# Optimization experiments

Measured on AMD Instinct MI355X. Metric: run time of the kernel, lower is better.

The kernel has to match this reference:

```python
import math
import jax, jax.numpy as jnp
import numpy as np

EMBED_DIM = 1024
NUM_HEADS = 16
HEAD_DIM = EMBED_DIM // NUM_HEADS
NUM_BUCKETS = 32
MAX_DISTANCE = 128


def _relative_position_bucket(relative_position, num_buckets=NUM_BUCKETS, max_distance=MAX_DISTANCE):
    # Bidirectional T5 bucketing (matches torch reference exactly).
    num_buckets = num_buckets // 2
    relative_buckets = (relative_position > 0).astype(jnp.int32) * num_buckets
    relative_position = jnp.abs(relative_position)
    max_exact = num_buckets // 2
    is_small = relative_position < max_exact
    rp_large = jnp.log(relative_position.astype(jnp.float32) / max_exact) / math.log(max_distance / max_exact)
    rp_large = max_exact + (rp_large * (num_buckets - max_exact)).astype(jnp.int32)
    rp_large = jnp.minimum(rp_large, num_buckets - 1)
    relative_buckets = relative_buckets + jnp.where(is_small, relative_position, rp_large)
    return relative_buckets


def compute_bias(rel_emb, query_length, key_length):
    context_position = jnp.arange(query_length, dtype=jnp.int32)[:, None]
    memory_position = jnp.arange(key_length, dtype=jnp.int32)[None, :]
    relative_position = memory_position - context_position  # [q, k]
    buckets = _relative_position_bucket(relative_position)
    values = rel_emb[buckets]                 # [q, k, h]
    return jnp.transpose(values, (2, 0, 1))[None]  # [1, h, q, k]


def setup_inputs() -> dict:
    key = jax.random.key(0)
    k1, k2, k3, k4 = jax.random.split(key, 4)
    B, S = 2, 2048
    hidden_states = jax.random.normal(k1, (B, S, EMBED_DIM), dtype=jnp.float32)
    scale = 1.0 / math.sqrt(EMBED_DIM)
    W_qkv = jax.random.normal(k2, (EMBED_DIM, 3 * EMBED_DIM), dtype=jnp.float32) * scale
    W_out = jax.random.normal(k3, (EMBED_DIM, EMBED_DIM), dtype=jnp.float32) * scale
    rel_emb = jax.random.normal(k4, (NUM_BUCKETS, NUM_HEADS), dtype=jnp.float32) * 0.02
    return {"hidden_states": hidden_states, "W_qkv": W_qkv, "W_out": W_out, "rel_emb": rel_emb}


def reference(hidden_states, W_qkv, W_out, rel_emb):
    B, S, _ = hidden_states.shape
    qkv = hidden_states @ W_qkv                                # [B, S, 3*D]
    qkv = qkv.reshape(B, S, 3, NUM_HEADS, HEAD_DIM)
    qkv = jnp.transpose(qkv, (0, 3, 2, 1, 4))                  # [B, H, 3, S, dh]
    q, k, v = qkv[:, :, 0], qkv[:, :, 1], qkv[:, :, 2]
    scores = jnp.einsum('bhqd,bhkd->bhqk', q, k)               # no 1/sqrt(d) scaling (T5 style)
    scores = scores + compute_bias(rel_emb, S, S)
    attn = jax.nn.softmax(scores.astype(jnp.float32), axis=-1).astype(scores.dtype)
    out = jnp.einsum('bhqk,bhkd->bhqd', attn, v)               # [B, H, S, dh]
    out = jnp.transpose(out, (0, 2, 1, 3)).reshape(B, S, EMBED_DIM)
    return out @ W_out
```

## Files before the change

### kernel.cpp

```cpp
#include <hip/hip_runtime.h>
#include <hip/hip_bf16.h>
#include <math.h>

typedef _Float16 f16;
typedef __attribute__((ext_vector_type(8))) _Float16 f16x8;
typedef __attribute__((ext_vector_type(4))) _Float16 f16x4;
typedef __attribute__((ext_vector_type(2))) _Float16 f16x2;
typedef __attribute__((ext_vector_type(4))) float f32x4;

#define EMBED 1024
#define NHEADS 16
#define HDIM 64
#define BATCH 2
#define SEQ 2048
#define BS 4096
#define LOG2E 1.4426950408889634f


__device__ __forceinline__ f32x4 mfma16x32(f16x8 a, f16x8 b, f32x4 c) {
  return __builtin_amdgcn_mfma_f32_16x16x32_f16(a, b, c, 0, 0, 0);
}
__device__ __forceinline__ f16x2 cvt_pk(float a, float b) {
  return __builtin_bit_cast(f16x2, __builtin_amdgcn_cvt_pkrtz(a, b));
}
__device__ __forceinline__ void gload_lds16(const f16* __restrict__ g, f16* l) {
  __builtin_amdgcn_global_load_lds(
      (const __attribute__((address_space(1))) void*)g,
      (__attribute__((address_space(3))) void*)l, 16, 0, 0);
}

__global__ void prep_kernel(const float* __restrict__ X, const float* __restrict__ Wqkv,
                            const float* __restrict__ Wout, const float* __restrict__ rel_emb,
                            f16* __restrict__ Xh, f16* __restrict__ Wqkv_t,
                            f16* __restrict__ Wout_t, float* __restrict__ btab) {
  __shared__ float tile[32][33];
  int bid = blockIdx.x, tid = threadIdx.x;
  if (bid < 4096) {
    int i = (bid * 256 + tid) * 4;
    float4 v = *(const float4*)(X + i);
    f16x4 o = { (f16)v.x, (f16)v.y, (f16)v.z, (f16)v.w };
    *(f16x4*)(Xh + i) = o;
  } else if (bid < 8192) {
    const float* in;
    f16* out;
    int N, idx;
    if (bid < 7168) { in = Wqkv; out = Wqkv_t; N = 3072; idx = bid - 4096; }
    else            { in = Wout; out = Wout_t; N = 1024; idx = bid - 7168; }
    int nt = N / 32;
    int n0 = (idx % nt) * 32, k0 = (idx / nt) * 32;
    int tx = tid & 31, ty = tid >> 5;
#pragma unroll
    for (int r = ty; r < 32; r += 8) tile[r][tx] = in[(size_t)(k0 + r) * N + n0 + tx];
    __syncthreads();
#pragma unroll
    for (int r = ty; r < 32; r += 8) out[(size_t)(n0 + r) * 1024 + k0 + tx] = (f16)tile[tx][r];
  } else {
    int idx = (bid - 8192) * 256 + tid;
    if (idx >= 4095) return;
    int rp = idx - 2047;
    int rb = rp > 0 ? 16 : 0;
    int arp = rp < 0 ? -rp : rp;
    int loc;
    if (arp < 8) {
      loc = arp;
    } else {
      float lr = logf((float)arp * 0.125f) * (1.0f / 2.7725887222397811f);
      int t = 8 + (int)(lr * 8.0f);
      loc = t < 15 ? t : 15;
    }
    int bucket = rb + loc;
#pragma unroll
    for (int h = 0; h < 16; h++) btab[h * 4095 + idx] = rel_emb[bucket * 16 + h] * LOG2E;
  }
}

__device__ __forceinline__ void gemm_core(const f16* __restrict__ A, const f16* __restrict__ Bt,
                                          int m0, int n0, int Kdim, f32x4 (&acc)[4][4]) {
  __shared__ __align__(16) f16 As[128 * 32];
  __shared__ __align__(16) f16 Bs[128 * 32];

  int tid = threadIdx.x;
  int lane = tid & 63, wave = tid >> 6;
  int l15 = lane & 15, quad = lane >> 4;
  int wr = (wave >> 1) * 64, wc = (wave & 1) * 64;
  int rowl = lane >> 2;
  int col8 = (lane & 3) * 8;

#pragma unroll
  for (int i = 0; i < 4; i++)
#pragma unroll
    for (int j = 0; j < 4; j++) acc[i][j] = f32x4{0.f, 0.f, 0.f, 0.f};

  for (int kt = 0; kt < Kdim / 32; kt++) {
    int kk = kt * 32;
#pragma unroll
    for (int c = 0; c < 2; c++) {
      int row = wave * 32 + c * 16 + rowl;
      gload_lds16(A + (size_t)(m0 + row) * Kdim + kk + col8, &As[(wave * 32 + c * 16) * 32]);
      gload_lds16(Bt + (size_t)(n0 + row) * Kdim + kk + col8, &Bs[(wave * 32 + c * 16) * 32]);
    }
    __syncthreads();
    f16x8 af[4], bf[4];
#pragma unroll
    for (int i = 0; i < 4; i++) af[i] = *(const f16x8*)(&As[(wr + i * 16 + l15) * 32 + quad * 8]);
#pragma unroll
    for (int j = 0; j < 4; j++) bf[j] = *(const f16x8*)(&Bs[(wc + j * 16 + l15) * 32 + quad * 8]);
#pragma unroll
    for (int i = 0; i < 4; i++)
#pragma unroll
      for (int j = 0; j < 4; j++) acc[i][j] = mfma16x32(af[i], bf[j], acc[i][j]);
    __syncthreads();
  }
}

__global__ __launch_bounds__(256, 3) void gemm_qkv_kernel(
    const f16* __restrict__ Xh, const f16* __restrict__ Wt,
    f16* __restrict__ Q, f16* __restrict__ Kp, f16* __restrict__ Vp) {
  f32x4 acc[4][4];
  int m0 = blockIdx.y * 128, n0 = blockIdx.x * 128;
  gemm_core(Xh, Wt, m0, n0, 1024, acc);

  int lane = threadIdx.x & 63, wave = threadIdx.x >> 6;
  int l15 = lane & 15, quad = lane >> 4;
  int wr = (wave >> 1) * 64, wc = (wave & 1) * 64;
  int nq = n0 + wc;
  int which = nq >> 10;
  int h = (nq >> 6) & 15;
  int b = m0 >> 11;
  int kt = ((m0 & 2047) + wr) >> 6;

  if (which == 2) {
    f16* vbase = Vp + (size_t)(b * 16 + h) * 131072 + (size_t)kt * 4096;
    int qr_lo = (quad >> 1);
    int joff = (quad & 1) * 4;
#pragma unroll
    for (int i = 0; i < 4; i++) {
      int cc = i >> 1;
      int qr = (i & 1) * 2 + qr_lo;
#pragma unroll
      for (int j = 0; j < 4; j++) {
        f16x4 pk = { (f16)acc[i][j][0], (f16)acc[i][j][1], (f16)acc[i][j][2], (f16)acc[i][j][3] };
        *(f16x4*)(vbase + (cc * 4 + j) * 512 + (qr * 16 + l15) * 8 + joff) = pk;
      }
    }
  } else if (which == 1) {
    f16* kbase = Kp + (size_t)(b * 16 + h) * 131072 + (size_t)kt * 4096;
    int jj = l15 & 7;
    int qk_half = l15 >> 3;
    int g = quad & 1;
    int hi2 = quad >> 1;
#pragma unroll
    for (int i = 0; i < 4; i++) {
      int cc = i >> 1;
      int m_hi = ((i & 1) * 2 + hi2) * 4;
#pragma unroll
      for (int j = 0; j < 4; j++) {
        int slot = (cc * 2 + g) * 2 + (j >> 1);
        int quadk = (j & 1) * 2 + qk_half;
#pragma unroll
        for (int r = 0; r < 4; r++) {
          kbase[slot * 512 + (quadk * 16 + m_hi + r) * 8 + jj] = (f16)acc[i][j][r];
        }
      }
    }
  } else {
#pragma unroll
    for (int i = 0; i < 4; i++) {
#pragma unroll
      for (int j = 0; j < 4; j++) {
        int d = j * 16 + l15;
#pragma unroll
        for (int r = 0; r < 4; r++) {
          int m = m0 + wr + i * 16 + quad * 4 + r;
          int s = m & 2047;
          Q[(((size_t)(b * 16 + h) * 2048 + s) << 6) + d] = (f16)(acc[i][j][r] * LOG2E);
        }
      }
    }
  }
}

__global__ __launch_bounds__(256, 4) void attn_kernel(
    const f16* __restrict__ Q, const f16* __restrict__ Kp, const f16* __restrict__ Vp,
    const float* __restrict__ btab, f16* __restrict__ O) {
  __shared__ float bias_lds[2112];

  int qt = blockIdx.x, bh = blockIdx.y;
  int qbase = qt * 64;
  int h = bh & 15, b = bh >> 4;
  int tid = threadIdx.x, lane = tid & 63, wave = tid >> 6;
  int l15 = lane & 15, quad = lane >> 4;

  const float* brow = btab + h * 4095 + (1984 - qbase);
  for (int i = tid; i < 2111; i += 256) bias_lds[i] = brow[i];

  const f16* qptr = Q + ((size_t)bh * 2048 + qbase + wave * 16 + l15) * 64 + quad * 8;
  f16x8 qf0 = *(const f16x8*)(qptr);
  f16x8 qf1 = *(const f16x8*)(qptr + 32);

  f32x4 accO[4] = {};
  float m_i = -INFINITY;
  float l_acc = 0.f;

  const f16* kbase = Kp + (size_t)bh * 131072 + 1792;
  const f16* vbase = Vp + (size_t)bh * 131072 + 1792;
  const int voff = lane * 8;
  const int bofs = quad * 8 - wave * 16 - l15 + 63;

  __syncthreads();

  auto do_tile = [&](const f16x8 (&kf)[8], const f16* vc, const float* bb) {
    f32x4 scT[4] = {};
#pragma unroll
    for (int c = 0; c < 4; c++) {
      scT[c] = mfma16x32(kf[c * 2 + 0], qf0, scT[c]);
      scT[c] = mfma16x32(kf[c * 2 + 1], qf1, scT[c]);
    }
    f16x8 vf[2][4];
#pragma unroll
    for (int cc = 0; cc < 2; cc++)
#pragma unroll
      for (int dblk = 0; dblk < 4; dblk++)
        vf[cc][dblk] = *(const f16x8*)(vc + ((cc * 4 + dblk) * 512 - 1792) + voff);
    scT[0] += f32x4{ bb[0],  bb[1],  bb[2],  bb[3]  };
    scT[1] += f32x4{ bb[4],  bb[5],  bb[6],  bb[7]  };
    scT[2] += f32x4{ bb[32], bb[33], bb[34], bb[35] };
    scT[3] += f32x4{ bb[36], bb[37], bb[38], bb[39] };
    float mp0 = fmaxf(fmaxf(fmaxf(scT[0][0], scT[0][1]), scT[0][2]), scT[0][3]);
    float mp1 = fmaxf(fmaxf(fmaxf(scT[1][0], scT[1][1]), scT[1][2]), scT[1][3]);
    float mp2 = fmaxf(fmaxf(fmaxf(scT[2][0], scT[2][1]), scT[2][2]), scT[2][3]);
    float mp3 = fmaxf(fmaxf(fmaxf(scT[3][0], scT[3][1]), scT[3][2]), scT[3][3]);
    float mp = fmaxf(fmaxf(fmaxf(mp0, mp1), mp2), mp3);
    if (__any(mp > m_i)) {
      float mx = fmaxf(mp, __shfl_xor(mp, 16));
      mx = fmaxf(mx, __shfl_xor(mx, 32));
      float mn = fmaxf(m_i, mx);
      float alpha = __builtin_amdgcn_exp2f(m_i - mn);
      m_i = mn;
      l_acc *= alpha;
      float arow[4];
#pragma unroll
      for (int r = 0; r < 4; r++) arow[r] = __shfl(alpha, quad * 4 + r);
#pragma unroll
      for (int d = 0; d < 4; d++)
#pragma unroll
        for (int r = 0; r < 4; r++) accO[d][r] *= arow[r];
    }
    float mx = m_i;
    f16x4 p[4];
#pragma unroll
    for (int c = 0; c < 4; c++) {
      float e0 = __builtin_amdgcn_exp2f(scT[c][0] - mx);
      float e1 = __builtin_amdgcn_exp2f(scT[c][1] - mx);
      float e2 = __builtin_amdgcn_exp2f(scT[c][2] - mx);
      float e3 = __builtin_amdgcn_exp2f(scT[c][3] - mx);
      l_acc += (e0 + e1) + (e2 + e3);
      f16x2 plo = cvt_pk(e0, e1);
      f16x2 phi = cvt_pk(e2, e3);
      p[c][0] = plo[0]; p[c][1] = plo[1]; p[c][2] = phi[0]; p[c][3] = phi[1];
    }
    f16x8 pp0 = __builtin_shufflevector(p[0], p[1], 0, 1, 2, 3, 4, 5, 6, 7);
    f16x8 pp1 = __builtin_shufflevector(p[2], p[3], 0, 1, 2, 3, 4, 5, 6, 7);
#pragma unroll
    for (int dblk = 0; dblk < 4; dblk++) accO[dblk] = mfma16x32(pp0, vf[0][dblk], accO[dblk]);
#pragma unroll
    for (int dblk = 0; dblk < 4; dblk++) accO[dblk] = mfma16x32(pp1, vf[1][dblk], accO[dblk]);
  };

  f16x8 k0[8], k1[8];
#pragma unroll
  for (int u = 0; u < 8; u++) k0[u] = *(const f16x8*)(kbase + (u * 512 - 1792) + voff);

  for (int ktp = 0; ktp < 16; ktp++) {
    int ktA = 2 * ktp, ktB = 2 * ktp + 1;
    const f16* kB = kbase + (size_t)ktB * 4096;
#pragma unroll
    for (int u = 0; u < 8; u++) k1[u] = *(const f16x8*)(kB + (u * 512 - 1792) + voff);
    do_tile(k0, vbase + (size_t)ktA * 4096, &bias_lds[ktA * 64 + bofs]);
    const f16* kC = kbase + (size_t)(ktB < 31 ? ktB + 1 : ktB) * 4096;
#pragma unroll
    for (int u = 0; u < 8; u++) k0[u] = *(const f16x8*)(kC + (u * 512 - 1792) + voff);
    do_tile(k1, vbase + (size_t)ktB * 4096, &bias_lds[ktB * 64 + bofs]);
  }

  float lt = l_acc;
  lt += __shfl_xor(lt, 16);
  lt += __shfl_xor(lt, 32);
  float linv = __builtin_amdgcn_rcpf(lt);
  float lrow[4];
#pragma unroll
  for (int r = 0; r < 4; r++) lrow[r] = __shfl(linv, quad * 4 + r);
#pragma unroll
  for (int dblk = 0; dblk < 4; dblk++) {
#pragma unroll
    for (int r = 0; r < 4; r++) {
      int q = qbase + wave * 16 + quad * 4 + r;
      O[((size_t)(b * 2048 + q) << 10) + h * 64 + dblk * 16 + l15] = (f16)(accO[dblk][r] * lrow[r]);
    }
  }
}

__global__ __launch_bounds__(256, 2) void gemm_out_kernel(
    const f16* __restrict__ Oh, const f16* __restrict__ Wt, float* __restrict__ out) {
  __shared__ __align__(16) f16 As[128 * 32];
  __shared__ __align__(16) f16 Bs[64 * 32];

  int tid = threadIdx.x;
  int lane = tid & 63, wave = tid >> 6;
  int l15 = lane & 15, quad = lane >> 4;
  int rowl = lane >> 2;
  int col8 = (lane & 3) * 8;
  int m0 = blockIdx.y * 128, n0 = blockIdx.x * 64;
  int wr = wave * 32;

  f32x4 acc[2][4];
#pragma unroll
  for (int i = 0; i < 2; i++)
#pragma unroll
    for (int j = 0; j < 4; j++) acc[i][j] = f32x4{0.f, 0.f, 0.f, 0.f};

  for (int kt = 0; kt < 32; kt++) {
    int kk = kt * 32;
#pragma unroll
    for (int c = 0; c < 2; c++) {
      int row = wave * 32 + c * 16 + rowl;
      gload_lds16(Oh + (size_t)(m0 + row) * 1024 + kk + col8, &As[(wave * 32 + c * 16) * 32]);
    }
    {
      int row = wave * 16 + rowl;
      gload_lds16(Wt + (size_t)(n0 + row) * 1024 + kk + col8, &Bs[(wave * 16) * 32]);
    }
    __syncthreads();
    f16x8 af[2], bf[4];
#pragma unroll
    for (int i = 0; i < 2; i++) af[i] = *(const f16x8*)(&As[(wr + i * 16 + l15) * 32 + quad * 8]);
#pragma unroll
    for (int j = 0; j < 4; j++) bf[j] = *(const f16x8*)(&Bs[(j * 16 + l15) * 32 + quad * 8]);
#pragma unroll
    for (int i = 0; i < 2; i++)
#pragma unroll
      for (int j = 0; j < 4; j++) acc[i][j] = mfma16x32(af[i], bf[j], acc[i][j]);
    __syncthreads();
  }

#pragma unroll
  for (int i = 0; i < 2; i++) {
#pragma unroll
    for (int j = 0; j < 4; j++) {
      int n = n0 + j * 16 + l15;
#pragma unroll
      for (int r = 0; r < 4; r++) {
        int m = m0 + wr + i * 16 + quad * 4 + r;
        out[((size_t)m << 10) + n] = acc[i][j][r];
      }
    }
  }
}

extern "C" void kernel_launch(void* const* d_in, const int* in_sizes, int n_in,
                              void* d_out, int out_size, void* d_ws, size_t ws_size,
                              hipStream_t stream) {
  const float* X = (const float*)d_in[0];
  const float* Wqkv = (const float*)d_in[1];
  const float* Wout = (const float*)d_in[2];
  const float* rel = (const float*)d_in[3];

  char* ws = (char*)d_ws;
  f16* Xh     = (f16*)(ws + 0);
  f16* Wqkv_t = (f16*)(ws + 8388608);
  f16* Wout_t = (f16*)(ws + 14680064);
  f16* Qw     = (f16*)(ws + 16777216);
  f16* Kp     = (f16*)(ws + 25165824);
  f16* Vp     = (f16*)(ws + 33554432);
  f16* Ow     = (f16*)(ws + 41943040);
  float* btab = (float*)(ws + 50331648);

  prep_kernel<<<8208, 256, 0, stream>>>(X, Wqkv, Wout, rel, Xh, Wqkv_t, Wout_t, btab);
  gemm_qkv_kernel<<<dim3(24, 32), 256, 0, stream>>>(Xh, Wqkv_t, Qw, Kp, Vp);
  attn_kernel<<<dim3(32, 32), 256, 0, stream>>>(Qw, Kp, Vp, btab, Ow);
  gemm_out_kernel<<<dim3(16, 32), 256, 0, stream>>>(Ow, Wout_t, (float*)d_out);
}
```

Measured before the change: 217.2 us.

## Split attention KV range across waves and merge partial softmax through LDS

```diff
diff --git a/kernel.cpp b/kernel.cpp
--- a/kernel.cpp
+++ b/kernel.cpp
@@ -15,6 +15,7 @@
 #define SEQ 2048
 #define BS 4096
 #define LOG2E 1.4426950408889634f
+#define NEG_BIG -3.0e38f
 
 
 __device__ __forceinline__ f32x4 mfma16x32(f16x8 a, f16x8 b, f32x4 c) {
@@ -180,122 +181,175 @@
   }
 }
 
-__global__ __launch_bounds__(256, 4) void attn_kernel(
+__global__ __launch_bounds__(256, 2) void attn_kernel(
     const f16* __restrict__ Q, const f16* __restrict__ Kp, const f16* __restrict__ Vp,
     const float* __restrict__ btab, f16* __restrict__ O) {
-  __shared__ float bias_lds[2112];
-
-  int qt = blockIdx.x, bh = blockIdx.y;
+  __shared__ float sbuf[2112];
+  __shared__ float obuf[4096];
+  __shared__ float mred[4][4][16];
+  __shared__ float lred[4][4][16];
+
+  int blk = blockIdx.x;
+  int bh = (blk & 7) * 4 + ((blk >> 3) & 3);
+  int qt = blk >> 5;
   int qbase = qt * 64;
   int h = bh & 15, b = bh >> 4;
   int tid = threadIdx.x, lane = tid & 63, wave = tid >> 6;
   int l15 = lane & 15, quad = lane >> 4;
 
   const float* brow = btab + h * 4095 + (1984 - qbase);
-  for (int i = tid; i < 2111; i += 256) bias_lds[i] = brow[i];
-
-  const f16* qptr = Q + ((size_t)bh * 2048 + qbase + wave * 16 + l15) * 64 + quad * 8;
-  f16x8 qf0 = *(const f16x8*)(qptr);
-  f16x8 qf1 = *(const f16x8*)(qptr + 32);
-
-  f32x4 accO[4] = {};
-  float m_i = -INFINITY;
-  float l_acc = 0.f;
+  for (int i = tid; i < 2111; i += 256) sbuf[i] = brow[i];
+
+  f16x8 qf[4][2];
+#pragma unroll
+  for (int g = 0; g < 4; g++) {
+    const f16* qptr = Q + ((size_t)bh * 2048 + qbase + g * 16 + l15) * 64 + quad * 8;
+    qf[g][0] = *(const f16x8*)(qptr);
+    qf[g][1] = *(const f16x8*)(qptr + 32);
+  }
+
+  f32x4 accO[4][4] = {};
+  float m_i[4], l_acc[4];
+#pragma unroll
+  for (int g = 0; g < 4; g++) { m_i[g] = NEG_BIG; l_acc[g] = 0.f; }
 
   const f16* kbase = Kp + (size_t)bh * 131072 + 1792;
   const f16* vbase = Vp + (size_t)bh * 131072 + 1792;
   const int voff = lane * 8;
-  const int bofs = quad * 8 - wave * 16 - l15 + 63;
 
   __syncthreads();
 
-  auto do_tile = [&](const f16x8 (&kf)[8], const f16* vc, const float* bb) {
-    f32x4 scT[4] = {};
-#pragma unroll
-    for (int c = 0; c < 4; c++) {
-      scT[c] = mfma16x32(kf[c * 2 + 0], qf0, scT[c]);
-      scT[c] = mfma16x32(kf[c * 2 + 1], qf1, scT[c]);
-    }
-    f16x8 vf[2][4];
-#pragma unroll
-    for (int cc = 0; cc < 2; cc++)
-#pragma unroll
-      for (int dblk = 0; dblk < 4; dblk++)
-        vf[cc][dblk] = *(const f16x8*)(vc + ((cc * 4 + dblk) * 512 - 1792) + voff);
-    scT[0] += f32x4{ bb[0],  bb[1],  bb[2],  bb[3]  };
-    scT[1] += f32x4{ bb[4],  bb[5],  bb[6],  bb[7]  };
-    scT[2] += f32x4{ bb[32], bb[33], bb[34], bb[35] };
-    scT[3] += f32x4{ bb[36], bb[37], bb[38], bb[39] };
-    float mp0 = fmaxf(fmaxf(fmaxf(scT[0][0], scT[0][1]), scT[0][2]), scT[0][3]);
-    float mp1 = fmaxf(fmaxf(fmaxf(scT[1][0], scT[1][1]), scT[1][2]), scT[1][3]);
-    float mp2 = fmaxf(fmaxf(fmaxf(scT[2][0], scT[2][1]), scT[2][2]), scT[2][3]);
-    float mp3 = fmaxf(fmaxf(fmaxf(scT[3][0], scT[3][1]), scT[3][2]), scT[3][3]);
-    float mp = fmaxf(fmaxf(fmaxf(mp0, mp1), mp2), mp3);
-    if (__any(mp > m_i)) {
-      float mx = fmaxf(mp, __shfl_xor(mp, 16));
-      mx = fmaxf(mx, __shfl_xor(mx, 32));
-      float mn = fmaxf(m_i, mx);
-      float alpha = __builtin_amdgcn_exp2f(m_i - mn);
-      m_i = mn;
-      l_acc *= alpha;
-      float arow[4];
-#pragma unroll
-      for (int r = 0; r < 4; r++) arow[r] = __shfl(alpha, quad * 4 + r);
-#pragma unroll
-      for (int d = 0; d < 4; d++)
-#pragma unroll
-        for (int r = 0; r < 4; r++) accO[d][r] *= arow[r];
-    }
-    float mx = m_i;
-    f16x4 p[4];
-#pragma unroll
-    for (int c = 0; c < 4; c++) {
-      float e0 = __builtin_amdgcn_exp2f(scT[c][0] - mx);
-      float e1 = __builtin_amdgcn_exp2f(scT[c][1] - mx);
-      float e2 = __builtin_amdgcn_exp2f(scT[c][2] - mx);
-      float e3 = __builtin_amdgcn_exp2f(scT[c][3] - mx);
-      l_acc += (e0 + e1) + (e2 + e3);
-      f16x2 plo = cvt_pk(e0, e1);
-      f16x2 phi = cvt_pk(e2, e3);
-      p[c][0] = plo[0]; p[c][1] = plo[1]; p[c][2] = phi[0]; p[c][3] = phi[1];
-    }
-    f16x8 pp0 = __builtin_shufflevector(p[0], p[1], 0, 1, 2, 3, 4, 5, 6, 7);
-    f16x8 pp1 = __builtin_shufflevector(p[2], p[3], 0, 1, 2, 3, 4, 5, 6, 7);
-#pragma unroll
-    for (int dblk = 0; dblk < 4; dblk++) accO[dblk] = mfma16x32(pp0, vf[0][dblk], accO[dblk]);
-#pragma unroll
-    for (int dblk = 0; dblk < 4; dblk++) accO[dblk] = mfma16x32(pp1, vf[1][dblk], accO[dblk]);
-  };
-
-  f16x8 k0[8], k1[8];
-#pragma unroll
-  for (int u = 0; u < 8; u++) k0[u] = *(const f16x8*)(kbase + (u * 512 - 1792) + voff);
-
-  for (int ktp = 0; ktp < 16; ktp++) {
-    int ktA = 2 * ktp, ktB = 2 * ktp + 1;
-    const f16* kB = kbase + (size_t)ktB * 4096;
-#pragma unroll
-    for (int u = 0; u < 8; u++) k1[u] = *(const f16x8*)(kB + (u * 512 - 1792) + voff);
-    do_tile(k0, vbase + (size_t)ktA * 4096, &bias_lds[ktA * 64 + bofs]);
-    const f16* kC = kbase + (size_t)(ktB < 31 ? ktB + 1 : ktB) * 4096;
-#pragma unroll
-    for (int u = 0; u < 8; u++) k0[u] = *(const f16x8*)(kC + (u * 512 - 1792) + voff);
-    do_tile(k1, vbase + (size_t)ktB * 4096, &bias_lds[ktB * 64 + bofs]);
-  }
-
-  float lt = l_acc;
-  lt += __shfl_xor(lt, 16);
-  lt += __shfl_xor(lt, 32);
-  float linv = __builtin_amdgcn_rcpf(lt);
+  for (int t = 0; t < 8; t++) {
+    int kt = t * 4 + wave;
+    const f16* kc = kbase + (size_t)kt * 4096;
+    const f16* vc = vbase + (size_t)kt * 4096;
+    f16x8 kf[8], vf[8];
+#pragma unroll
+    for (int u = 0; u < 8; u++) kf[u] = *(const f16x8*)(kc + (u * 512 - 1792) + voff);
+#pragma unroll
+    for (int u = 0; u < 8; u++) vf[u] = *(const f16x8*)(vc + (u * 512 - 1792) + voff);
+    const float* btile = &sbuf[kt * 64 + quad * 8 - l15 + 63];
+
+#pragma unroll
+    for (int g = 0; g < 4; g++) {
+      const float* bb = btile - g * 16;
+      f32x4 scT[4] = {};
+#pragma unroll
+      for (int c = 0; c < 4; c++) {
+        scT[c] = mfma16x32(kf[c * 2 + 0], qf[g][0], scT[c]);
+        scT[c] = mfma16x32(kf[c * 2 + 1], qf[g][1], scT[c]);
+      }
+      scT[0] += f32x4{ bb[0],  bb[1],  bb[2],  bb[3]  };
+      scT[1] += f32x4{ bb[4],  bb[5],  bb[6],  bb[7]  };
+      scT[2] += f32x4{ bb[32], bb[33], bb[34], bb[35] };
+      scT[3] += f32x4{ bb[36], bb[37], bb[38], bb[39] };
+      float mp0 = fmaxf(fmaxf(fmaxf(scT[0][0], scT[0][1]), scT[0][2]), scT[0][3]);
+      float mp1 = fmaxf(fmaxf(fmaxf(scT[1][0], scT[1][1]), scT[1][2]), scT[1][3]);
+      float mp2 = fmaxf(fmaxf(fmaxf(scT[2][0], scT[2][1]), scT[2][2]), scT[2][3]);
+      float mp3 = fmaxf(fmaxf(fmaxf(scT[3][0], scT[3][1]), scT[3][2]), scT[3][3]);
+      float mp = fmaxf(fmaxf(fmaxf(mp0, mp1), mp2), mp3);
+      if (__any(mp > m_i[g])) {
+        float mx = fmaxf(mp, __shfl_xor(mp, 16));
+        mx = fmaxf(mx, __shfl_xor(mx, 32));
+        float mn = fmaxf(m_i[g], mx);
+        float alpha = __builtin_amdgcn_exp2f(m_i[g] - mn);
+        m_i[g] = mn;
+        l_acc[g] *= alpha;
+        float arow[4];
+#pragma unroll
+        for (int r = 0; r < 4; r++) arow[r] = __shfl(alpha, quad * 4 + r);
+#pragma unroll
+        for (int d = 0; d < 4; d++)
+#pragma unroll
+          for (int r = 0; r < 4; r++) accO[g][d][r] *= arow[r];
+      }
+      float mx = m_i[g];
+      f16x4 p[4];
+#pragma unroll
+      for (int c = 0; c < 4; c++) {
+        float e0 = __builtin_amdgcn_exp2f(scT[c][0] - mx);
+        float e1 = __builtin_amdgcn_exp2f(scT[c][1] - mx);
+        float e2 = __builtin_amdgcn_exp2f(scT[c][2] - mx);
+        float e3 = __builtin_amdgcn_exp2f(scT[c][3] - mx);
+        l_acc[g] += (e0 + e1) + (e2 + e3);
+        f16x2 plo = cvt_pk(e0, e1);
+        f16x2 phi = cvt_pk(e2, e3);
+        p[c][0] = plo[0]; p[c][1] = plo[1]; p[c][2] = phi[0]; p[c][3] = phi[1];
+      }
+      f16x8 pp0 = __builtin_shufflevector(p[0], p[1], 0, 1, 2, 3, 4, 5, 6, 7);
+      f16x8 pp1 = __builtin_shufflevector(p[2], p[3], 0, 1, 2, 3, 4, 5, 6, 7);
+#pragma unroll
+      for (int dblk = 0; dblk < 4; dblk++) accO[g][dblk] = mfma16x32(pp0, vf[dblk], accO[g][dblk]);
+#pragma unroll
+      for (int dblk = 0; dblk < 4; dblk++) accO[g][dblk] = mfma16x32(pp1, vf[4 + dblk], accO[g][dblk]);
+    }
+  }
+
+#pragma unroll
+  for (int g = 0; g < 4; g++) {
+    l_acc[g] += __shfl_xor(l_acc[g], 16);
+    l_acc[g] += __shfl_xor(l_acc[g], 32);
+  }
+
+  if (quad == 0) {
+#pragma unroll
+    for (int g = 0; g < 4; g++) {
+      mred[g][wave][l15] = m_i[g];
+      lred[g][wave][l15] = l_acc[g];
+    }
+  }
+  __syncthreads();
+
+  float alpha[4], linvG[4];
+#pragma unroll
+  for (int g = 0; g < 4; g++) {
+    float a0 = mred[g][0][l15], a1 = mred[g][1][l15];
+    float a2 = mred[g][2][l15], a3 = mred[g][3][l15];
+    float ms = fmaxf(fmaxf(a0, a1), fmaxf(a2, a3));
+    float ls = __builtin_amdgcn_exp2f(a0 - ms) * lred[g][0][l15]
+             + __builtin_amdgcn_exp2f(a1 - ms) * lred[g][1][l15]
+             + __builtin_amdgcn_exp2f(a2 - ms) * lred[g][2][l15]
+             + __builtin_amdgcn_exp2f(a3 - ms) * lred[g][3][l15];
+    alpha[g] = __builtin_amdgcn_exp2f(m_i[g] - ms);
+    linvG[g] = 1.0f / ls;
+  }
+#pragma unroll
+  for (int g = 0; g < 4; g++) {
+    float arow[4];
+#pragma unroll
+    for (int r = 0; r < 4; r++) arow[r] = __shfl(alpha[g], quad * 4 + r);
+#pragma unroll
+    for (int d = 0; d < 4; d++)
+#pragma unroll
+      for (int r = 0; r < 4; r++) accO[g][d][r] *= arow[r];
+  }
+#pragma unroll
+  for (int w = 0; w < 4; w++) {
+    if (wave == w) {
+#pragma unroll
+      for (int g = 0; g < 4; g++)
+#pragma unroll
+        for (int dblk = 0; dblk < 4; dblk++)
+#pragma unroll
+          for (int r = 0; r < 4; r++) {
+            int idx = (g * 16 + quad * 4 + r) * 64 + dblk * 16 + l15;
+            if (w == 0) obuf[idx] = accO[g][dblk][r];
+            else        obuf[idx] += accO[g][dblk][r];
+          }
+    }
+    __syncthreads();
+  }
+  float lw = wave == 0 ? linvG[0] : wave == 1 ? linvG[1] : wave == 2 ? linvG[2] : linvG[3];
   float lrow[4];
 #pragma unroll
-  for (int r = 0; r < 4; r++) lrow[r] = __shfl(linv, quad * 4 + r);
+  for (int r = 0; r < 4; r++) lrow[r] = __shfl(lw, quad * 4 + r);
 #pragma unroll
   for (int dblk = 0; dblk < 4; dblk++) {
 #pragma unroll
     for (int r = 0; r < 4; r++) {
-      int q = qbase + wave * 16 + quad * 4 + r;
-      O[((size_t)(b * 2048 + q) << 10) + h * 64 + dblk * 16 + l15] = (f16)(accO[dblk][r] * lrow[r]);
+      int ql = wave * 16 + quad * 4 + r;
+      float val = obuf[ql * 64 + dblk * 16 + l15] * lrow[r];
+      O[((size_t)(b * 2048 + qbase + ql) << 10) + h * 64 + dblk * 16 + l15] = (f16)val;
     }
   }
 }
@@ -377,6 +431,6 @@
 
   prep_kernel<<<8208, 256, 0, stream>>>(X, Wqkv, Wout, rel, Xh, Wqkv_t, Wout_t, btab);
   gemm_qkv_kernel<<<dim3(24, 32), 256, 0, stream>>>(Xh, Wqkv_t, Qw, Kp, Vp);
-  attn_kernel<<<dim3(32, 32), 256, 0, stream>>>(Qw, Kp, Vp, btab, Ow);
+  attn_kernel<<<1024, 256, 0, stream>>>(Qw, Kp, Vp, btab, Ow);
   gemm_out_kernel<<<dim3(16, 32), 256, 0, stream>>>(Ow, Wout_t, (float*)d_out);
 }
```

Measured after the change: 204.9 us. 1.06x faster.
